# Kernel optimization log

Hardware: AMD Instinct MI355X
Metric: run time of the kernel (lower is better)

The kernel has to match this reference:

```python
import jax, jax.numpy as jnp
import numpy as np

B = 2_000_000
HID = 50
DIM = 2


def setup_inputs() -> dict:
    key = jax.random.key(0)
    k_y, k_w1, k_w2 = jax.random.split(key, 3)
    y = jax.random.normal(k_y, (B, DIM), dtype=jnp.float32)
    # weights ~ N(0, 0.1), biases = 0, matching the torch init
    W1 = 0.1 * jax.random.normal(k_w1, (HID, DIM), dtype=jnp.float32)
    b1 = jnp.zeros((HID,), dtype=jnp.float32)
    W2 = 0.1 * jax.random.normal(k_w2, (DIM, HID), dtype=jnp.float32)
    b2 = jnp.zeros((DIM,), dtype=jnp.float32)
    t = jnp.float32(0.0)
    return {"t": t, "y": y, "W1": W1, "b1": b1, "W2": W2, "b2": b2}


def reference(t, y, W1, b1, W2, b2):
    # Linear(2->50) + tanh + Linear(50->2); t is unused by the ODE func body.
    h = jnp.tanh(y @ W1.T + b1)  # [B, 50]
    return h @ W2.T + b2          # [B, 2]
```

## Files before the change

### kernel.cpp

```cpp
#include <hip/hip_runtime.h>


typedef float f32x2 __attribute__((ext_vector_type(2)));

#define NROWS 2000000
#define HID 50
#define C2L 2.8853900817779268f

__global__ void prep_kernel(const float* __restrict__ W1, const float* __restrict__ b1,
                            const float* __restrict__ W2, const float* __restrict__ b2,
                            float* __restrict__ w) {
    const int j = threadIdx.x;
    float wa = 0.f, wb = 0.f, wc = 0.f, va = 0.f, vb = 0.f;
    float t0 = 0.f, t1 = 0.f;
    if (j < HID) {
        wa = W1[2 * j] * C2L;
        wb = W1[2 * j + 1] * C2L;
        wc = b1[j] * C2L;
        t0 = W2[j];
        t1 = W2[HID + j];
        va = -2.0f * t0;
        vb = -2.0f * t1;
    }
    if (j < 56) {
        w[2 * j] = wa;        w[2 * j + 1] = wa;
        w[128 + 2 * j] = wb;  w[128 + 2 * j + 1] = wb;
        w[256 + 2 * j] = wc;  w[256 + 2 * j + 1] = wc;
        w[384 + 2 * j] = va;  w[384 + 2 * j + 1] = va;
        w[512 + 2 * j] = vb;  w[512 + 2 * j + 1] = vb;
    }
#pragma unroll
    for (int off = 32; off > 0; off >>= 1) {
        t0 += __shfl_down(t0, off, 64);
        t1 += __shfl_down(t1, off, 64);
    }
    if (j == 0) { w[640] = b2[0] + t0; w[641] = b2[1] + t1; }
}

__global__ __launch_bounds__(256) void ode_main(const float* __restrict__ y,
                                                const float* __restrict__ w,
                                                float* __restrict__ out) {
    const int tid = blockIdx.x * 256 + threadIdx.x;
    if (tid >= NROWS / 2) return;

    const float4 yv = reinterpret_cast<const float4*>(y)[tid];
    const f32x2 ya = {yv.x, yv.z};
    const f32x2 yb = {yv.y, yv.w};

    f32x2 o0 = {w[640], w[640]};
    f32x2 o1 = {w[641], w[641]};

    const f32x2* wa2 = (const f32x2*)(w);
    const f32x2* wb2 = (const f32x2*)(w + 128);
    const f32x2* wc2 = (const f32x2*)(w + 256);
    const f32x2* va2 = (const f32x2*)(w + 384);
    const f32x2* vb2 = (const f32x2*)(w + 512);

#pragma unroll
    for (int j = 0; j < 56; ++j) {
        f32x2 z = __builtin_elementwise_fma(
            wa2[j], ya, __builtin_elementwise_fma(wb2[j], yb, wc2[j]));
        f32x2 e;
        e.x = __builtin_amdgcn_exp2f(z.x);
        e.y = __builtin_amdgcn_exp2f(z.y);
        f32x2 ep = e + (f32x2){1.0f, 1.0f};
        f32x2 r;
        r.x = __builtin_amdgcn_rcpf(ep.x);
        r.y = __builtin_amdgcn_rcpf(ep.y);
        o0 = __builtin_elementwise_fma(va2[j], r, o0);
        o1 = __builtin_elementwise_fma(vb2[j], r, o1);
    }

    float4 s; s.x = o0.x; s.y = o1.x; s.z = o0.y; s.w = o1.y;
    reinterpret_cast<float4*>(out)[tid] = s;
}

extern "C" void kernel_launch(void* const* d_in, const int* in_sizes, int n_in,
                              void* d_out, int out_size, void* d_ws, size_t ws_size,
                              hipStream_t stream) {
    const float* y  = (const float*)d_in[1];
    const float* W1 = (const float*)d_in[2];
    const float* b1 = (const float*)d_in[3];
    const float* W2 = (const float*)d_in[4];
    const float* b2 = (const float*)d_in[5];
    float* out = (float*)d_out;
    float* w   = (float*)d_ws;

    prep_kernel<<<1, 64, 0, stream>>>(W1, b1, W2, b2, w);

    const int threads = NROWS / 2;
    const int grid = (threads + 255) / 256;
    ode_main<<<grid, 256, 0, stream>>>(y, w, out);
}
```

Before: 102.4 us.

## Fuse weight prep into main kernel and batch reciprocals via Montgomery trick

Removes the separate prep kernel launch by having each block compute the transformed weights into LDS, followed by a barrier. It trims the padded hidden loop from 56 to 52 units. The main loop now groups 8 sigmoid denominators and inverts them with a single rcp plus prefix products (Montgomery batch inversion), trading transcendental rcp ops for extra multiplies. Risks include overflow or underflow in the product of eight (1+exp) terms when inputs are large, and redundant per-block weight loads plus a sync.

Result: faster. 99.32 us (-3.0%).

```diff
diff --git a/kernel.cpp b/kernel.cpp
--- a/kernel.cpp
+++ b/kernel.cpp
@@ -5,70 +5,132 @@
 
 #define NROWS 2000000
 #define HID 50
+#define NJ 52
 #define C2L 2.8853900817779268f
 
-__global__ void prep_kernel(const float* __restrict__ W1, const float* __restrict__ b1,
-                            const float* __restrict__ W2, const float* __restrict__ b2,
-                            float* __restrict__ w) {
-    const int j = threadIdx.x;
-    float wa = 0.f, wb = 0.f, wc = 0.f, va = 0.f, vb = 0.f;
-    float t0 = 0.f, t1 = 0.f;
-    if (j < HID) {
-        wa = W1[2 * j] * C2L;
-        wb = W1[2 * j + 1] * C2L;
-        wc = b1[j] * C2L;
-        t0 = W2[j];
-        t1 = W2[HID + j];
-        va = -2.0f * t0;
-        vb = -2.0f * t1;
+__global__ __launch_bounds__(256) void ode_fused(const float* __restrict__ y,
+                                                 const float* __restrict__ W1,
+                                                 const float* __restrict__ b1,
+                                                 const float* __restrict__ W2,
+                                                 const float* __restrict__ b2,
+                                                 float* __restrict__ out) {
+    __shared__ float lds[642];
+
+    const int tid = blockIdx.x * 256 + threadIdx.x;
+
+    if (threadIdx.x < 64) {
+        const int j = threadIdx.x;
+        float wa = 0.f, wb = 0.f, wc = 0.f, va = 0.f, vb = 0.f;
+        float t0 = 0.f, t1 = 0.f;
+        if (j < HID) {
+            wa = W1[2 * j] * C2L;
+            wb = W1[2 * j + 1] * C2L;
+            wc = b1[j] * C2L;
+            t0 = W2[j];
+            t1 = W2[HID + j];
+            va = -2.0f * t0;
+            vb = -2.0f * t1;
+        }
+        if (j < NJ) {
+            lds[2 * j] = wa;        lds[2 * j + 1] = wa;
+            lds[128 + 2 * j] = wb;  lds[128 + 2 * j + 1] = wb;
+            lds[256 + 2 * j] = wc;  lds[256 + 2 * j + 1] = wc;
+            lds[384 + 2 * j] = va;  lds[384 + 2 * j + 1] = va;
+            lds[512 + 2 * j] = vb;  lds[512 + 2 * j + 1] = vb;
+        }
+#pragma unroll
+        for (int off = 32; off > 0; off >>= 1) {
+            t0 += __shfl_down(t0, off, 64);
+            t1 += __shfl_down(t1, off, 64);
+        }
+        if (j == 0) { lds[640] = b2[0] + t0; lds[641] = b2[1] + t1; }
     }
-    if (j < 56) {
-        w[2 * j] = wa;        w[2 * j + 1] = wa;
-        w[128 + 2 * j] = wb;  w[128 + 2 * j + 1] = wb;
-        w[256 + 2 * j] = wc;  w[256 + 2 * j + 1] = wc;
-        w[384 + 2 * j] = va;  w[384 + 2 * j + 1] = va;
-        w[512 + 2 * j] = vb;  w[512 + 2 * j + 1] = vb;
-    }
-#pragma unroll
-    for (int off = 32; off > 0; off >>= 1) {
-        t0 += __shfl_down(t0, off, 64);
-        t1 += __shfl_down(t1, off, 64);
-    }
-    if (j == 0) { w[640] = b2[0] + t0; w[641] = b2[1] + t1; }
-}
+    __syncthreads();
 
-__global__ __launch_bounds__(256) void ode_main(const float* __restrict__ y,
-                                                const float* __restrict__ w,
-                                                float* __restrict__ out) {
-    const int tid = blockIdx.x * 256 + threadIdx.x;
     if (tid >= NROWS / 2) return;
 
     const float4 yv = reinterpret_cast<const float4*>(y)[tid];
     const f32x2 ya = {yv.x, yv.z};
     const f32x2 yb = {yv.y, yv.w};
 
-    f32x2 o0 = {w[640], w[640]};
-    f32x2 o1 = {w[641], w[641]};
+    f32x2 o0 = {lds[640], lds[640]};
+    f32x2 o1 = {lds[641], lds[641]};
 
-    const f32x2* wa2 = (const f32x2*)(w);
-    const f32x2* wb2 = (const f32x2*)(w + 128);
-    const f32x2* wc2 = (const f32x2*)(w + 256);
-    const f32x2* va2 = (const f32x2*)(w + 384);
-    const f32x2* vb2 = (const f32x2*)(w + 512);
+    const f32x2* wa2 = (const f32x2*)(lds);
+    const f32x2* wb2 = (const f32x2*)(lds + 128);
+    const f32x2* wc2 = (const f32x2*)(lds + 256);
+    const f32x2* va2 = (const f32x2*)(lds + 384);
+    const f32x2* vb2 = (const f32x2*)(lds + 512);
+
+    const f32x2 one = {1.0f, 1.0f};
 
 #pragma unroll
-    for (int j = 0; j < 56; ++j) {
-        f32x2 z = __builtin_elementwise_fma(
-            wa2[j], ya, __builtin_elementwise_fma(wb2[j], yb, wc2[j]));
-        f32x2 e;
-        e.x = __builtin_amdgcn_exp2f(z.x);
-        e.y = __builtin_amdgcn_exp2f(z.y);
-        f32x2 ep = e + (f32x2){1.0f, 1.0f};
-        f32x2 r;
-        r.x = __builtin_amdgcn_rcpf(ep.x);
-        r.y = __builtin_amdgcn_rcpf(ep.y);
-        o0 = __builtin_elementwise_fma(va2[j], r, o0);
-        o1 = __builtin_elementwise_fma(vb2[j], r, o1);
+    for (int grp = 0; grp < 6; ++grp) {
+        const int j0 = grp * 8;
+        f32x2 d[8];
+#pragma unroll
+        for (int k = 0; k < 8; ++k) {
+            f32x2 z = __builtin_elementwise_fma(wa2[j0 + k], ya,
+                       __builtin_elementwise_fma(wb2[j0 + k], yb, wc2[j0 + k]));
+            f32x2 e;
+            e.x = __builtin_amdgcn_exp2f(z.x);
+            e.y = __builtin_amdgcn_exp2f(z.y);
+            d[k] = e + one;
+        }
+        f32x2 f1 = d[0] * d[1];
+        f32x2 f2 = f1 * d[2];
+        f32x2 f3 = f2 * d[3];
+        f32x2 f4 = f3 * d[4];
+        f32x2 f5 = f4 * d[5];
+        f32x2 f6 = f5 * d[6];
+        f32x2 f7 = f6 * d[7];
+        f32x2 g;
+        g.x = __builtin_amdgcn_rcpf(f7.x);
+        g.y = __builtin_amdgcn_rcpf(f7.y);
+        f32x2 r[8];
+        r[7] = f6 * g;  g = g * d[7];
+        r[6] = f5 * g;  g = g * d[6];
+        r[5] = f4 * g;  g = g * d[5];
+        r[4] = f3 * g;  g = g * d[4];
+        r[3] = f2 * g;  g = g * d[3];
+        r[2] = f1 * g;  g = g * d[2];
+        r[1] = d[0] * g; g = g * d[1];
+        r[0] = g;
+#pragma unroll
+        for (int k = 0; k < 8; ++k) {
+            o0 = __builtin_elementwise_fma(va2[j0 + k], r[k], o0);
+            o1 = __builtin_elementwise_fma(vb2[j0 + k], r[k], o1);
+        }
+    }
+
+    {
+        const int j0 = 48;
+        f32x2 d[4];
+#pragma unroll
+        for (int k = 0; k < 4; ++k) {
+            f32x2 z = __builtin_elementwise_fma(wa2[j0 + k], ya,
+                       __builtin_elementwise_fma(wb2[j0 + k], yb, wc2[j0 + k]));
+            f32x2 e;
+            e.x = __builtin_amdgcn_exp2f(z.x);
+            e.y = __builtin_amdgcn_exp2f(z.y);
+            d[k] = e + one;
+        }
+        f32x2 f1 = d[0] * d[1];
+        f32x2 f2 = f1 * d[2];
+        f32x2 f3 = f2 * d[3];
+        f32x2 g;
+        g.x = __builtin_amdgcn_rcpf(f3.x);
+        g.y = __builtin_amdgcn_rcpf(f3.y);
+        f32x2 r[4];
+        r[3] = f2 * g;  g = g * d[3];
+        r[2] = f1 * g;  g = g * d[2];
+        r[1] = d[0] * g; g = g * d[1];
+        r[0] = g;
+#pragma unroll
+        for (int k = 0; k < 4; ++k) {
+            o0 = __builtin_elementwise_fma(va2[j0 + k], r[k], o0);
+            o1 = __builtin_elementwise_fma(vb2[j0 + k], r[k], o1);
+        }
     }
 
     float4 s; s.x = o0.x; s.y = o1.x; s.z = o0.y; s.w = o1.y;
@@ -84,11 +146,8 @@
     const float* W2 = (const float*)d_in[4];
     const float* b2 = (const float*)d_in[5];
     float* out = (float*)d_out;
-    float* w   = (float*)d_ws;
-
-    prep_kernel<<<1, 64, 0, stream>>>(W1, b1, W2, b2, w);
 
     const int threads = NROWS / 2;
     const int grid = (threads + 255) / 256;
-    ode_main<<<grid, 256, 0, stream>>>(y, w, out);
+    ode_fused<<<grid, 256, 0, stream>>>(y, W1, b1, W2, b2, out);
 }
```

## Fuse weight prep into main kernel and batch reciprocals four at a time

Applied to the files above, without the earlier changes.

Folds the single-block weight preprocessing kernel into the main kernel. Each block now builds the scaled weights in shared memory behind a barrier, which removes one launch and the global workspace round trip. The 52-unit hidden loop is regrouped into 13 groups of four. Each group uses one shared reciprocal of the product of four denominators plus multiplies in place of four separate rcp instructions, trading transcendental throughput for extra multiplies. Risks include overflow or underflow in the product of four exp terms, redundant per-block weight setup, and the barrier cost.

New measurement: 98.10 us. 1.04x faster.

```diff
diff --git a/kernel.cpp b/kernel.cpp
--- a/kernel.cpp
+++ b/kernel.cpp
@@ -5,70 +5,106 @@
 
 #define NROWS 2000000
 #define HID 50
+#define NGRP 13
 #define C2L 2.8853900817779268f
 
-__global__ void prep_kernel(const float* __restrict__ W1, const float* __restrict__ b1,
-                            const float* __restrict__ W2, const float* __restrict__ b2,
-                            float* __restrict__ w) {
-    const int j = threadIdx.x;
-    float wa = 0.f, wb = 0.f, wc = 0.f, va = 0.f, vb = 0.f;
-    float t0 = 0.f, t1 = 0.f;
-    if (j < HID) {
-        wa = W1[2 * j] * C2L;
-        wb = W1[2 * j + 1] * C2L;
-        wc = b1[j] * C2L;
-        t0 = W2[j];
-        t1 = W2[HID + j];
-        va = -2.0f * t0;
-        vb = -2.0f * t1;
+__global__ __launch_bounds__(256, 8) void ode_fused(const float* __restrict__ y,
+                                                    const float* __restrict__ W1,
+                                                    const float* __restrict__ b1,
+                                                    const float* __restrict__ W2,
+                                                    const float* __restrict__ b2,
+                                                    float* __restrict__ out) {
+    __shared__ float lds[NGRP * 40 + 2];
+
+    const int tid = blockIdx.x * 256 + threadIdx.x;
+
+    if (threadIdx.x < 64) {
+        const int j = threadIdx.x;
+        float wa = 0.f, wb = 0.f, wc = 0.f, va = 0.f, vb = 0.f;
+        float t0 = 0.f, t1 = 0.f;
+        if (j < HID) {
+            wa = W1[2 * j] * C2L;
+            wb = W1[2 * j + 1] * C2L;
+            wc = b1[j] * C2L;
+            t0 = W2[j];
+            t1 = W2[HID + j];
+            va = -2.0f * t0;
+            vb = -2.0f * t1;
+        }
+        if (j < NGRP * 4) {
+            const int base = (j >> 2) * 40 + 2 * (j & 3);
+            lds[base +  0] = wa; lds[base +  1] = wa;
+            lds[base +  8] = wb; lds[base +  9] = wb;
+            lds[base + 16] = wc; lds[base + 17] = wc;
+            lds[base + 24] = va; lds[base + 25] = va;
+            lds[base + 32] = vb; lds[base + 33] = vb;
+        }
+#pragma unroll
+        for (int off = 32; off > 0; off >>= 1) {
+            t0 += __shfl_down(t0, off, 64);
+            t1 += __shfl_down(t1, off, 64);
+        }
+        if (j == 0) { lds[NGRP * 40] = b2[0] + t0; lds[NGRP * 40 + 1] = b2[1] + t1; }
     }
-    if (j < 56) {
-        w[2 * j] = wa;        w[2 * j + 1] = wa;
-        w[128 + 2 * j] = wb;  w[128 + 2 * j + 1] = wb;
-        w[256 + 2 * j] = wc;  w[256 + 2 * j + 1] = wc;
-        w[384 + 2 * j] = va;  w[384 + 2 * j + 1] = va;
-        w[512 + 2 * j] = vb;  w[512 + 2 * j + 1] = vb;
-    }
-#pragma unroll
-    for (int off = 32; off > 0; off >>= 1) {
-        t0 += __shfl_down(t0, off, 64);
-        t1 += __shfl_down(t1, off, 64);
-    }
-    if (j == 0) { w[640] = b2[0] + t0; w[641] = b2[1] + t1; }
-}
+    __syncthreads();
 
-__global__ __launch_bounds__(256) void ode_main(const float* __restrict__ y,
-                                                const float* __restrict__ w,
-                                                float* __restrict__ out) {
-    const int tid = blockIdx.x * 256 + threadIdx.x;
     if (tid >= NROWS / 2) return;
 
     const float4 yv = reinterpret_cast<const float4*>(y)[tid];
     const f32x2 ya = {yv.x, yv.z};
     const f32x2 yb = {yv.y, yv.w};
 
-    f32x2 o0 = {w[640], w[640]};
-    f32x2 o1 = {w[641], w[641]};
+    f32x2 o0 = {lds[NGRP * 40], lds[NGRP * 40]};
+    f32x2 o1 = {lds[NGRP * 40 + 1], lds[NGRP * 40 + 1]};
 
-    const f32x2* wa2 = (const f32x2*)(w);
-    const f32x2* wb2 = (const f32x2*)(w + 128);
-    const f32x2* wc2 = (const f32x2*)(w + 256);
-    const f32x2* va2 = (const f32x2*)(w + 384);
-    const f32x2* vb2 = (const f32x2*)(w + 512);
+    const f32x2 one = {1.0f, 1.0f};
 
 #pragma unroll
-    for (int j = 0; j < 56; ++j) {
-        f32x2 z = __builtin_elementwise_fma(
-            wa2[j], ya, __builtin_elementwise_fma(wb2[j], yb, wc2[j]));
-        f32x2 e;
-        e.x = __builtin_amdgcn_exp2f(z.x);
-        e.y = __builtin_amdgcn_exp2f(z.y);
-        f32x2 ep = e + (f32x2){1.0f, 1.0f};
-        f32x2 r;
-        r.x = __builtin_amdgcn_rcpf(ep.x);
-        r.y = __builtin_amdgcn_rcpf(ep.y);
-        o0 = __builtin_elementwise_fma(va2[j], r, o0);
-        o1 = __builtin_elementwise_fma(vb2[j], r, o1);
+    for (int g = 0; g < NGRP; ++g) {
+        const float4* Q = (const float4*)(lds + g * 40);
+        const float4 A0 = Q[0], A1 = Q[1];
+        const float4 B0 = Q[2], B1 = Q[3];
+        const float4 C0 = Q[4], C1 = Q[5];
+        const float4 V0 = Q[6], V1 = Q[7];
+        const float4 U0 = Q[8], U1 = Q[9];
+
+        f32x2 z0 = __builtin_elementwise_fma((f32x2){A0.x, A0.y}, ya,
+                    __builtin_elementwise_fma((f32x2){B0.x, B0.y}, yb, (f32x2){C0.x, C0.y}));
+        f32x2 z1 = __builtin_elementwise_fma((f32x2){A0.z, A0.w}, ya,
+                    __builtin_elementwise_fma((f32x2){B0.z, B0.w}, yb, (f32x2){C0.z, C0.w}));
+        f32x2 z2 = __builtin_elementwise_fma((f32x2){A1.x, A1.y}, ya,
+                    __builtin_elementwise_fma((f32x2){B1.x, B1.y}, yb, (f32x2){C1.x, C1.y}));
+        f32x2 z3 = __builtin_elementwise_fma((f32x2){A1.z, A1.w}, ya,
+                    __builtin_elementwise_fma((f32x2){B1.z, B1.w}, yb, (f32x2){C1.z, C1.w}));
+
+        f32x2 d0, d1, d2, d3;
+        d0.x = __builtin_amdgcn_exp2f(z0.x); d0.y = __builtin_amdgcn_exp2f(z0.y);
+        d1.x = __builtin_amdgcn_exp2f(z1.x); d1.y = __builtin_amdgcn_exp2f(z1.y);
+        d2.x = __builtin_amdgcn_exp2f(z2.x); d2.y = __builtin_amdgcn_exp2f(z2.y);
+        d3.x = __builtin_amdgcn_exp2f(z3.x); d3.y = __builtin_amdgcn_exp2f(z3.y);
+        d0 = d0 + one; d1 = d1 + one; d2 = d2 + one; d3 = d3 + one;
+
+        f32x2 p01 = d0 * d1;
+        f32x2 p23 = d2 * d3;
+        f32x2 f = p01 * p23;
+        f32x2 gg;
+        gg.x = __builtin_amdgcn_rcpf(f.x);
+        gg.y = __builtin_amdgcn_rcpf(f.y);
+        f32x2 g01 = gg * p23;
+        f32x2 g23 = gg * p01;
+        f32x2 r0 = g01 * d1;
+        f32x2 r1 = g01 * d0;
+        f32x2 r2 = g23 * d3;
+        f32x2 r3 = g23 * d2;
+
+        o0 = __builtin_elementwise_fma((f32x2){V0.x, V0.y}, r0, o0);
+        o1 = __builtin_elementwise_fma((f32x2){U0.x, U0.y}, r0, o1);
+        o0 = __builtin_elementwise_fma((f32x2){V0.z, V0.w}, r1, o0);
+        o1 = __builtin_elementwise_fma((f32x2){U0.z, U0.w}, r1, o1);
+        o0 = __builtin_elementwise_fma((f32x2){V1.x, V1.y}, r2, o0);
+        o1 = __builtin_elementwise_fma((f32x2){U1.x, U1.y}, r2, o1);
+        o0 = __builtin_elementwise_fma((f32x2){V1.z, V1.w}, r3, o0);
+        o1 = __builtin_elementwise_fma((f32x2){U1.z, U1.w}, r3, o1);
     }
 
     float4 s; s.x = o0.x; s.y = o1.x; s.z = o0.y; s.w = o1.y;
@@ -84,11 +120,8 @@
     const float* W2 = (const float*)d_in[4];
     const float* b2 = (const float*)d_in[5];
     float* out = (float*)d_out;
-    float* w   = (float*)d_ws;
-
-    prep_kernel<<<1, 64, 0, stream>>>(W1, b1, W2, b2, w);
 
     const int threads = NROWS / 2;
     const int grid = (threads + 255) / 256;
-    ode_main<<<grid, 256, 0, stream>>>(y, w, out);
+    ode_fused<<<grid, 256, 0, stream>>>(y, W1, b1, W2, b2, out);
 }
```
